# Kernel optimization log

Measured on AMD Instinct MI355X. Metric: run time of the kernel, lower is better.

The kernel has to match this reference:

```python
import jax, jax.numpy as jnp
import numpy as np

T, B, H, IN = 512, 128, 1024, 64  # IN = input_dim (x_feat=63 plus 1 feedback channel)
INIT_OUT = 1e-9


def setup_inputs() -> dict:
    key = jax.random.key(0)
    ks = jax.random.split(key, 8)
    s_ih = 1.0 / np.sqrt(H)
    return {
        "x": jax.random.normal(ks[0], (T, B, IN - 1), dtype=jnp.float32),
        # torch nn.LSTM params, gate order i,f,g,o stacked along dim 0
        "W_ih": jax.random.uniform(ks[1], (4 * H, IN), dtype=jnp.float32, minval=-s_ih, maxval=s_ih),
        "W_hh": jax.random.uniform(ks[2], (4 * H, H), dtype=jnp.float32, minval=-s_ih, maxval=s_ih),
        "b_ih": jax.random.uniform(ks[3], (4 * H,), dtype=jnp.float32, minval=-s_ih, maxval=s_ih),
        "b_hh": jax.random.uniform(ks[4], (4 * H,), dtype=jnp.float32, minval=-s_ih, maxval=s_ih),
        # nn.Linear(hidden_dim, 1)
        "W_lin": jax.random.uniform(ks[5], (1, H), dtype=jnp.float32, minval=-s_ih, maxval=s_ih),
        "b_lin": jax.random.uniform(ks[6], (1,), dtype=jnp.float32, minval=-s_ih, maxval=s_ih),
    }


def _forward(x, W_ih, W_hh, b_ih, b_hh, W_lin, b_lin):
    b = b_ih + b_hh

    def step(carry, xt):
        h, c, prev_out = carry  # h,c: (B,H); prev_out: (B,)
        inp = jnp.concatenate([xt, prev_out[:, None]], axis=1)  # (B, IN)
        gates = inp @ W_ih.T + h @ W_hh.T + b                   # (B, 4H)
        i, f, g, o = jnp.split(gates, 4, axis=1)
        c = jax.nn.sigmoid(f) * c + jax.nn.sigmoid(i) * jnp.tanh(g)
        h = jax.nn.sigmoid(o) * jnp.tanh(c)
        out = (h @ W_lin.T + b_lin)[:, 0]                        # (B,)
        return (h, c, out), out

    h0 = jnp.zeros((B, H), x.dtype)
    c0 = jnp.zeros((B, H), x.dtype)
    out0 = jnp.full((B,), INIT_OUT, x.dtype)
    _, outs = jax.lax.scan(step, (h0, c0, out0), x[1:])          # (T-1, B)
    return jnp.concatenate([out0[None, :], outs], axis=0)        # (T, B)


def reference(x, W_ih, W_hh, b_ih, b_hh, W_lin, b_lin):
    return _forward(x, W_ih, W_hh, b_ih, b_hh, W_lin, b_lin)
```

## Files before the change

### kernel.cpp

```cpp
#include <hip/hip_runtime.h>
#include <stdint.h>


typedef short short8 __attribute__((ext_vector_type(8)));
typedef float float4v __attribute__((ext_vector_type(4)));
typedef int int4v __attribute__((ext_vector_type(4)));

#define KP 1152

__device__ __forceinline__ unsigned short f2bf(float f) {
  unsigned int u = __float_as_uint(f);
  u += 0x7fffu + ((u >> 16) & 1u);
  return (unsigned short)(u >> 16);
}
__device__ __forceinline__ float sigm(float x) { return 1.0f / (1.0f + __expf(-x)); }
__device__ __forceinline__ float tanh_f(float x) {
  float ax = fabsf(x);
  float e = __expf(-2.0f * ax);
  float r = (1.0f - e) / (1.0f + e);
  return x < 0.0f ? -r : r;
}

__global__ void prep_w(const float* __restrict__ W_ih, const float* __restrict__ W_hh,
                       const float* __restrict__ W_lin, const float* __restrict__ b_ih,
                       const float* __restrict__ b_hh, const float* __restrict__ b_lin,
                       unsigned short* __restrict__ Wcat, float* __restrict__ b1,
                       float* __restrict__ b2) {
  int idx = blockIdx.x * 256 + threadIdx.x;
  if (idx < 4096 * KP) {
    int j = idx / KP;
    int k = idx - j * KP;
    float v = 0.0f;
    if (k < 63) v = W_ih[j * 64 + k];
    else if (k >= 64 && k < 1088) {
      int kk = k - 64;
      v = W_hh[j * 1024 + kk] + W_ih[j * 64 + 63] * W_lin[kk];
    }
    Wcat[idx] = f2bf(v);
  }
  if (idx < 4096) {
    float wfb = W_ih[idx * 64 + 63];
    float base = b_ih[idx] + b_hh[idx];
    b1[idx] = base + 1e-9f * wfb;
    b2[idx] = base + b_lin[0] * wfb;
  }
}

__global__ void prep_x(const float* __restrict__ x, unsigned short* __restrict__ xbf) {
  int idx = blockIdx.x * 256 + threadIdx.x;
  int c = idx & 63;
  int bi = idx >> 6;
  unsigned short v = 0;
  if (c < 63) v = f2bf(x[bi * 63 + c]);
  xbf[idx] = v;
}

__global__ void initk(unsigned int* __restrict__ Hz, int* __restrict__ flags) {
  int idx = blockIdx.x * 256 + threadIdx.x;
  Hz[idx] = 0u;
  Hz[idx + 65536] = 0u;
  if (idx < 1024) flags[idx] = 0;
}

__global__ __launch_bounds__(256, 1) void lstm_rec(
    const unsigned short* __restrict__ Wcat, const unsigned short* __restrict__ xbf,
    const float* __restrict__ b1, const float* __restrict__ b2,
    const float* __restrict__ Wlin, unsigned short* __restrict__ Hbuf,
    float* __restrict__ outp, int* __restrict__ flags) {
  const int tid = threadIdx.x;
  const int bid = blockIdx.x;
  const int g = bid & 7;
  const int mb = bid >> 3;
  const int wv = tid >> 6;
  const int ln = tid & 63;
  const int lr = ln & 15;
  const int lq = ln >> 4;
  const int rp = wv * 2 + (ln >> 5);
  const int c = ln & 31;

  __shared__ __align__(16) float pbuf[2][4][8][16][20];

  short8 bf[8][9];
#pragma unroll
  for (int n = 0; n < 8; ++n) {
    const unsigned short* wrow =
        Wcat + (size_t)((n >> 1) * 1024 + mb * 32 + (n & 1) * 16 + lr) * KP;
#pragma unroll
    for (int j = 0; j < 9; ++j)
      bf[n][j] = *reinterpret_cast<const short8*>(wrow + (wv * 9 + j) * 32 + lq * 8);
  }
#pragma unroll
  for (int n = 0; n < 8; ++n)
#pragma unroll
    for (int j = 0; j < 9; ++j)
      asm volatile("" : "+v"(bf[n][j]));

  const int kb = wv * 9;
  const int jlo = (kb < 2) ? 2 : 0;
  const int jhi = (kb + 9 > 34) ? 7 : 9;
  const int pmin = (kb < 2) ? 0 : kb - 2;
  const int pmax = (kb + 6 < 31) ? kb + 6 : 31;
  const int cnt = 4 * (pmax - pmin + 1);
  const int* fp = flags + g * 128 + 4 * pmin + ((ln < cnt) ? ln : cnt - 1);

  int hoff[9];
#pragma unroll
  for (int j = 0; j < 9; ++j)
    hoff[j] = ((g * 16 + lr) * 1024 + (kb + j - 2) * 32 + lq * 8) * 2;

  const int gcb = mb * 32 + c;
  float bias2[4];
#pragma unroll
  for (int q = 0; q < 4; ++q) bias2[q] = b2[q * 1024 + gcb];
  const float wl = Wlin[gcb];
  float cs0 = 0.f, cs1 = 0.f;

  for (int t = 1; t < 512; ++t) {
    const int tm1 = t - 1;
    short8 xa0, xa1;
    if (kb == 0) {
      const unsigned short* xrow =
          xbf + (size_t)t * 8192 + (g * 16 + lr) * 64 + lq * 8;
      xa0 = *reinterpret_cast<const short8*>(xrow);
      xa1 = *reinterpret_cast<const short8*>(xrow + 32);
    }

    if (t > 1) {
      int guard = 0;
      for (;;) {
        int v;
        asm volatile("global_load_dword %0, %1, off sc0 sc1\n\ts_waitcnt vmcnt(0)"
                     : "=v"(v) : "v"(fp) : "memory");
        if (__all(v >= tm1)) break;
        if (++guard > (1 << 18)) break;
      }
    }

    const unsigned short* hb = Hbuf + ((t - 1) & 1) * 131072;
    short8 af[9];
    if (kb == 0) { af[0] = xa0; af[1] = xa1; }
    if (jhi == 7) {
      short8 z8 = {0, 0, 0, 0, 0, 0, 0, 0};
      af[7] = z8; af[8] = z8;
    }
#pragma unroll
    for (int j = 0; j < 9; ++j)
      if (j >= jlo && j < jhi)
        asm volatile("global_load_dwordx4 %0, %1, %2 sc0 sc1"
                     : "=v"(af[j]) : "v"(hoff[j]), "s"(hb));
    asm volatile("s_waitcnt vmcnt(0)" ::: "memory");
    __builtin_amdgcn_sched_barrier(0);

    float4v acc[8];
#pragma unroll
    for (int n = 0; n < 8; ++n) acc[n] = (float4v){0.f, 0.f, 0.f, 0.f};
#pragma unroll
    for (int j = 0; j < 9; ++j)
#pragma unroll
      for (int n = 0; n < 8; ++n)
        acc[n] = __builtin_amdgcn_mfma_f32_16x16x32_bf16(af[j], bf[n][j], acc[n], 0, 0, 0);

#pragma unroll
    for (int n = 0; n < 8; ++n)
      *reinterpret_cast<float4v*>(&pbuf[t & 1][wv][n][lr][lq * 4]) = acc[n];
    __syncthreads();

    float ga0[4], ga1[4];
    const int nlo = c >> 4;
    const int cc = c & 15;
#pragma unroll
    for (int q = 0; q < 4; ++q) {
      float s0 = 0.f, s1 = 0.f;
#pragma unroll
      for (int w2 = 0; w2 < 4; ++w2) {
        const float* pp = &pbuf[t & 1][w2][q * 2 + nlo][cc][2 * rp];
        s0 += pp[0];
        s1 += pp[1];
      }
      ga0[q] = s0;
      ga1[q] = s1;
    }
    float lb0 = bias2[0], lb1 = bias2[1], lb2 = bias2[2], lb3 = bias2[3];
    if (t == 1) {
      lb0 = b1[gcb];
      lb1 = b1[1024 + gcb];
      lb2 = b1[2048 + gcb];
      lb3 = b1[3072 + gcb];
    }
    float i0 = sigm(ga0[0] + lb0), f0 = sigm(ga0[1] + lb1);
    float G0 = tanh_f(ga0[2] + lb2), o0 = sigm(ga0[3] + lb3);
    float i1 = sigm(ga1[0] + lb0), f1 = sigm(ga1[1] + lb1);
    float G1 = tanh_f(ga1[2] + lb2), o1 = sigm(ga1[3] + lb3);
    cs0 = f0 * cs0 + i0 * G0;
    cs1 = f1 * cs1 + i1 * G1;
    float h0v = o0 * tanh_f(cs0);
    float h1v = o1 * tanh_f(cs1);

    unsigned short* Hd = Hbuf + (t & 1) * 131072;
    const int r0 = g * 16 + rp * 2;
    unsigned short* p0 = Hd + (size_t)r0 * 1024 + gcb;
    unsigned short* p1 = p0 + 1024;
    int hb0 = (int)f2bf(h0v), hb1 = (int)f2bf(h1v);
    asm volatile("global_store_short %0, %1, off sc0 sc1" :: "v"(p0), "v"(hb0) : "memory");
    asm volatile("global_store_short %0, %1, off sc0 sc1" :: "v"(p1), "v"(hb1) : "memory");
    asm volatile("s_waitcnt vmcnt(0)" ::: "memory");
    if (ln == 0) {
      int* fp2 = flags + g * 128 + mb * 4 + wv;
      asm volatile("global_store_dword %0, %1, off sc0 sc1" :: "v"(fp2), "v"(t) : "memory");
    }

    float pa = h0v * wl, pb = h1v * wl;
    pa += __shfl_xor(pa, 1); pb += __shfl_xor(pb, 1);
    pa += __shfl_xor(pa, 2); pb += __shfl_xor(pb, 2);
    pa += __shfl_xor(pa, 4); pb += __shfl_xor(pb, 4);
    pa += __shfl_xor(pa, 8); pb += __shfl_xor(pb, 8);
    pa += __shfl_xor(pa, 16); pb += __shfl_xor(pb, 16);
    if (c == 0) {
      outp[(size_t)(t * 128 + r0) * 32 + mb] = pa;
      outp[(size_t)(t * 128 + r0 + 1) * 32 + mb] = pb;
    }
  }
}

__global__ void finalize(const float* __restrict__ outp, const float* __restrict__ b_lin,
                         float* __restrict__ out) {
  int tid = threadIdx.x;
  int ln = tid & 63;
  int wv = tid >> 6;
  int half = ln >> 5;
  int lane = ln & 31;
  int row = blockIdx.x * 8 + wv * 2 + half;
  float v = outp[(size_t)row * 32 + lane];
  v += __shfl_xor(v, 1);
  v += __shfl_xor(v, 2);
  v += __shfl_xor(v, 4);
  v += __shfl_xor(v, 8);
  v += __shfl_xor(v, 16);
  if (lane == 0) out[row] = (row < 128) ? 1e-9f : (v + b_lin[0]);
}

extern "C" void kernel_launch(void* const* d_in, const int* in_sizes, int n_in,
                              void* d_out, int out_size, void* d_ws, size_t ws_size,
                              hipStream_t stream) {
  const float* x = (const float*)d_in[0];
  const float* W_ih = (const float*)d_in[1];
  const float* W_hh = (const float*)d_in[2];
  const float* b_ih = (const float*)d_in[3];
  const float* b_hh = (const float*)d_in[4];
  const float* W_lin = (const float*)d_in[5];
  const float* b_lin = (const float*)d_in[6];
  float* out = (float*)d_out;

  char* ws = (char*)d_ws;
  const size_t WS_WCAT = 0;
  const size_t WS_XBF  = 9437184;
  const size_t WS_B1   = 17825792;
  const size_t WS_B2   = 17842176;
  const size_t WS_H    = 17858560;
  const size_t WS_OUTP = 18382848;
  const size_t WS_FLAG = 26771456;
  if (ws_size < WS_FLAG + 4096) return;

  unsigned short* Wcat = (unsigned short*)(ws + WS_WCAT);
  unsigned short* xbf = (unsigned short*)(ws + WS_XBF);
  float* b1 = (float*)(ws + WS_B1);
  float* b2 = (float*)(ws + WS_B2);
  unsigned short* Hbuf = (unsigned short*)(ws + WS_H);
  float* outp = (float*)(ws + WS_OUTP);
  int* flags = (int*)(ws + WS_FLAG);

  prep_w<<<18432, 256, 0, stream>>>(W_ih, W_hh, W_lin, b_ih, b_hh, b_lin, Wcat, b1, b2);
  prep_x<<<16384, 256, 0, stream>>>(x, xbf);
  initk<<<256, 256, 0, stream>>>((unsigned int*)Hbuf, flags);
  lstm_rec<<<256, 256, 0, stream>>>(Wcat, xbf, b1, b2, W_lin, Hbuf, outp, flags);
  finalize<<<8192, 256, 0, stream>>>(outp, b_lin, out);
}
```

Baseline: 2.086 ms.

## Split recurrent LSTM kernel across 512 blocks with 16 hidden columns each

Halves the hidden-column slice per block (16 instead of 32) and launches 512 persistent blocks at two per CU instead of 256 at one. Each wave then holds half the weight fragments and issues half the MFMAs per step, so two co-resident blocks can overlap each other's latency and spin-waits. The flag array doubles and pollers read two flags per lane. The partial-output buffer widens to 64 slices, with finalize adjusted to match. This relies on all 512 blocks being co-resident for the spin barrier and adds more flag traffic per step.

```diff
diff --git a/kernel.cpp b/kernel.cpp
--- a/kernel.cpp
+++ b/kernel.cpp
@@ -5,6 +5,7 @@
 typedef short short8 __attribute__((ext_vector_type(8)));
 typedef float float4v __attribute__((ext_vector_type(4)));
 typedef int int4v __attribute__((ext_vector_type(4)));
+typedef int int2v __attribute__((ext_vector_type(2)));
 
 #define KP 1152
 
@@ -59,10 +60,10 @@
   int idx = blockIdx.x * 256 + threadIdx.x;
   Hz[idx] = 0u;
   Hz[idx + 65536] = 0u;
-  if (idx < 1024) flags[idx] = 0;
-}
-
-__global__ __launch_bounds__(256, 1) void lstm_rec(
+  if (idx < 2048) flags[idx] = 0;
+}
+
+__global__ __launch_bounds__(256, 2) void lstm_rec(
     const unsigned short* __restrict__ Wcat, const unsigned short* __restrict__ xbf,
     const float* __restrict__ b1, const float* __restrict__ b2,
     const float* __restrict__ Wlin, unsigned short* __restrict__ Hbuf,
@@ -75,22 +76,21 @@
   const int ln = tid & 63;
   const int lr = ln & 15;
   const int lq = ln >> 4;
-  const int rp = wv * 2 + (ln >> 5);
-  const int c = ln & 31;
-
-  __shared__ __align__(16) float pbuf[2][4][8][16][20];
-
-  short8 bf[8][9];
-#pragma unroll
-  for (int n = 0; n < 8; ++n) {
-    const unsigned short* wrow =
-        Wcat + (size_t)((n >> 1) * 1024 + mb * 32 + (n & 1) * 16 + lr) * KP;
+  const int prow = tid >> 4;
+  const int pcol = tid & 15;
+
+  __shared__ __align__(16) float pbuf[2][4][4][16][20];
+
+  short8 bf[4][9];
+#pragma unroll
+  for (int n = 0; n < 4; ++n) {
+    const unsigned short* wrow = Wcat + (size_t)(n * 1024 + mb * 16 + lr) * KP;
 #pragma unroll
     for (int j = 0; j < 9; ++j)
       bf[n][j] = *reinterpret_cast<const short8*>(wrow + (wv * 9 + j) * 32 + lq * 8);
   }
 #pragma unroll
-  for (int n = 0; n < 8; ++n)
+  for (int n = 0; n < 4; ++n)
 #pragma unroll
     for (int j = 0; j < 9; ++j)
       asm volatile("" : "+v"(bf[n][j]));
@@ -98,22 +98,23 @@
   const int kb = wv * 9;
   const int jlo = (kb < 2) ? 2 : 0;
   const int jhi = (kb + 9 > 34) ? 7 : 9;
-  const int pmin = (kb < 2) ? 0 : kb - 2;
-  const int pmax = (kb + 6 < 31) ? kb + 6 : 31;
-  const int cnt = 4 * (pmax - pmin + 1);
-  const int* fp = flags + g * 128 + 4 * pmin + ((ln < cnt) ? ln : cnt - 1);
+  const int cmin = (kb < 2) ? 0 : kb - 2;
+  const int cmax = (kb + 6 < 31) ? kb + 6 : 31;
+  const int cnt = 8 * (cmax - cmin + 1);
+  const int half = cnt >> 1;
+  const int* fp = flags + g * 256 + 8 * cmin + 2 * ((ln < half) ? ln : half - 1);
 
   int hoff[9];
 #pragma unroll
   for (int j = 0; j < 9; ++j)
     hoff[j] = ((g * 16 + lr) * 1024 + (kb + j - 2) * 32 + lq * 8) * 2;
 
-  const int gcb = mb * 32 + c;
+  const int gcb = mb * 16 + pcol;
   float bias2[4];
 #pragma unroll
   for (int q = 0; q < 4; ++q) bias2[q] = b2[q * 1024 + gcb];
   const float wl = Wlin[gcb];
-  float cs0 = 0.f, cs1 = 0.f;
+  float cs = 0.f;
 
   for (int t = 1; t < 512; ++t) {
     const int tm1 = t - 1;
@@ -128,10 +129,10 @@
     if (t > 1) {
       int guard = 0;
       for (;;) {
-        int v;
-        asm volatile("global_load_dword %0, %1, off sc0 sc1\n\ts_waitcnt vmcnt(0)"
-                     : "=v"(v) : "v"(fp) : "memory");
-        if (__all(v >= tm1)) break;
+        int2v ff;
+        asm volatile("global_load_dwordx2 %0, %1, off sc0 sc1\n\ts_waitcnt vmcnt(0)"
+                     : "=v"(ff) : "v"(fp) : "memory");
+        if (__all((ff.x >= tm1) && (ff.y >= tm1))) break;
         if (++guard > (1 << 18)) break;
       }
     }
@@ -151,34 +152,25 @@
     asm volatile("s_waitcnt vmcnt(0)" ::: "memory");
     __builtin_amdgcn_sched_barrier(0);
 
-    float4v acc[8];
-#pragma unroll
-    for (int n = 0; n < 8; ++n) acc[n] = (float4v){0.f, 0.f, 0.f, 0.f};
-#pragma unroll
-    for (int j = 0; j < 9; ++j)
-#pragma unroll
-      for (int n = 0; n < 8; ++n)
+    float4v acc[4];
+#pragma unroll
+    for (int n = 0; n < 4; ++n) acc[n] = (float4v){0.f, 0.f, 0.f, 0.f};
+#pragma unroll
+    for (int j = 0; j < 9; ++j)
+#pragma unroll
+      for (int n = 0; n < 4; ++n)
         acc[n] = __builtin_amdgcn_mfma_f32_16x16x32_bf16(af[j], bf[n][j], acc[n], 0, 0, 0);
 
 #pragma unroll
-    for (int n = 0; n < 8; ++n)
+    for (int n = 0; n < 4; ++n)
       *reinterpret_cast<float4v*>(&pbuf[t & 1][wv][n][lr][lq * 4]) = acc[n];
     __syncthreads();
 
-    float ga0[4], ga1[4];
-    const int nlo = c >> 4;
-    const int cc = c & 15;
+    float ga[4];
 #pragma unroll
     for (int q = 0; q < 4; ++q) {
-      float s0 = 0.f, s1 = 0.f;
-#pragma unroll
-      for (int w2 = 0; w2 < 4; ++w2) {
-        const float* pp = &pbuf[t & 1][w2][q * 2 + nlo][cc][2 * rp];
-        s0 += pp[0];
-        s1 += pp[1];
-      }
-      ga0[q] = s0;
-      ga1[q] = s1;
+      const float* pp0 = &pbuf[t & 1][0][q][pcol][prow];
+      ga[q] = pp0[0] + pp0[4 * 16 * 20] + pp0[2 * 4 * 16 * 20] + pp0[3 * 4 * 16 * 20];
     }
     float lb0 = bias2[0], lb1 = bias2[1], lb2 = bias2[2], lb3 = bias2[3];
     if (t == 1) {
@@ -187,38 +179,28 @@
       lb2 = b1[2048 + gcb];
       lb3 = b1[3072 + gcb];
     }
-    float i0 = sigm(ga0[0] + lb0), f0 = sigm(ga0[1] + lb1);
-    float G0 = tanh_f(ga0[2] + lb2), o0 = sigm(ga0[3] + lb3);
-    float i1 = sigm(ga1[0] + lb0), f1 = sigm(ga1[1] + lb1);
-    float G1 = tanh_f(ga1[2] + lb2), o1 = sigm(ga1[3] + lb3);
-    cs0 = f0 * cs0 + i0 * G0;
-    cs1 = f1 * cs1 + i1 * G1;
-    float h0v = o0 * tanh_f(cs0);
-    float h1v = o1 * tanh_f(cs1);
+    float iv = sigm(ga[0] + lb0), fv = sigm(ga[1] + lb1);
+    float Gv = tanh_f(ga[2] + lb2), ov = sigm(ga[3] + lb3);
+    cs = fv * cs + iv * Gv;
+    float hv = ov * tanh_f(cs);
 
     unsigned short* Hd = Hbuf + (t & 1) * 131072;
-    const int r0 = g * 16 + rp * 2;
-    unsigned short* p0 = Hd + (size_t)r0 * 1024 + gcb;
-    unsigned short* p1 = p0 + 1024;
-    int hb0 = (int)f2bf(h0v), hb1 = (int)f2bf(h1v);
+    unsigned short* p0 = Hd + (size_t)(g * 16 + prow) * 1024 + gcb;
+    int hb0 = (int)f2bf(hv);
     asm volatile("global_store_short %0, %1, off sc0 sc1" :: "v"(p0), "v"(hb0) : "memory");
-    asm volatile("global_store_short %0, %1, off sc0 sc1" :: "v"(p1), "v"(hb1) : "memory");
     asm volatile("s_waitcnt vmcnt(0)" ::: "memory");
     if (ln == 0) {
-      int* fp2 = flags + g * 128 + mb * 4 + wv;
+      int* fp2 = flags + g * 256 + mb * 4 + wv;
       asm volatile("global_store_dword %0, %1, off sc0 sc1" :: "v"(fp2), "v"(t) : "memory");
     }
 
-    float pa = h0v * wl, pb = h1v * wl;
-    pa += __shfl_xor(pa, 1); pb += __shfl_xor(pb, 1);
-    pa += __shfl_xor(pa, 2); pb += __shfl_xor(pb, 2);
-    pa += __shfl_xor(pa, 4); pb += __shfl_xor(pb, 4);
-    pa += __shfl_xor(pa, 8); pb += __shfl_xor(pb, 8);
-    pa += __shfl_xor(pa, 16); pb += __shfl_xor(pb, 16);
-    if (c == 0) {
-      outp[(size_t)(t * 128 + r0) * 32 + mb] = pa;
-      outp[(size_t)(t * 128 + r0 + 1) * 32 + mb] = pb;
-    }
+    float pa = hv * wl;
+    pa += __shfl_xor(pa, 1);
+    pa += __shfl_xor(pa, 2);
+    pa += __shfl_xor(pa, 4);
+    pa += __shfl_xor(pa, 8);
+    if (pcol == 0)
+      outp[(size_t)(t * 128 + g * 16 + prow) * 64 + mb] = pa;
   }
 }
 
@@ -227,16 +209,15 @@
   int tid = threadIdx.x;
   int ln = tid & 63;
   int wv = tid >> 6;
-  int half = ln >> 5;
-  int lane = ln & 31;
-  int row = blockIdx.x * 8 + wv * 2 + half;
-  float v = outp[(size_t)row * 32 + lane];
+  int row = blockIdx.x * 4 + wv;
+  float v = outp[(size_t)row * 64 + ln];
   v += __shfl_xor(v, 1);
   v += __shfl_xor(v, 2);
   v += __shfl_xor(v, 4);
   v += __shfl_xor(v, 8);
   v += __shfl_xor(v, 16);
-  if (lane == 0) out[row] = (row < 128) ? 1e-9f : (v + b_lin[0]);
+  v += __shfl_xor(v, 32);
+  if (ln == 0) out[row] = (row < 128) ? 1e-9f : (v + b_lin[0]);
 }
 
 extern "C" void kernel_launch(void* const* d_in, const int* in_sizes, int n_in,
@@ -258,8 +239,8 @@
   const size_t WS_B2   = 17842176;
   const size_t WS_H    = 17858560;
   const size_t WS_OUTP = 18382848;
-  const size_t WS_FLAG = 26771456;
-  if (ws_size < WS_FLAG + 4096) return;
+  const size_t WS_END  = 35160064;
+  if (ws_size < WS_END) return;
 
   unsigned short* Wcat = (unsigned short*)(ws + WS_WCAT);
   unsigned short* xbf = (unsigned short*)(ws + WS_XBF);
@@ -267,11 +248,11 @@
   float* b2 = (float*)(ws + WS_B2);
   unsigned short* Hbuf = (unsigned short*)(ws + WS_H);
   float* outp = (float*)(ws + WS_OUTP);
-  int* flags = (int*)(ws + WS_FLAG);
+  int* flags = (int*)(ws + WS_OUTP);
 
   prep_w<<<18432, 256, 0, stream>>>(W_ih, W_hh, W_lin, b_ih, b_hh, b_lin, Wcat, b1, b2);
   prep_x<<<16384, 256, 0, stream>>>(x, xbf);
   initk<<<256, 256, 0, stream>>>((unsigned int*)Hbuf, flags);
-  lstm_rec<<<256, 256, 0, stream>>>(Wcat, xbf, b1, b2, W_lin, Hbuf, outp, flags);
-  finalize<<<8192, 256, 0, stream>>>(outp, b_lin, out);
-}
+  lstm_rec<<<512, 256, 0, stream>>>(Wcat, xbf, b1, b2, W_lin, Hbuf, outp, flags);
+  finalize<<<16384, 256, 0, stream>>>(outp, b_lin, out);
+}
```

Result: slower. 4.371 ms (+109.5%).

## Retile LSTM recurrence to 32-row batch groups with LDS-resident weight slices

Applied to the files above, without the earlier changes.

Changes the persistent recurrent kernel's work split. Each of the 256 blocks now covers 32 batch rows by 16 hidden columns across all four gates, instead of 16 rows by 32 columns. Most W_hh tiles move into shared memory, with the input weights and tail tiles kept in registers. Each B fragment read from LDS now feeds two MFMAs, one per 16-row half, which is meant to cut weight register pressure and make better use of each loaded weight. The cost is per-step LDS reads, more hidden-state loads per block, a second barrier per step, and a wider partial-output buffer that shares workspace with the flag array.

```diff
diff --git a/kernel.cpp b/kernel.cpp
--- a/kernel.cpp
+++ b/kernel.cpp
@@ -69,60 +69,83 @@
     float* __restrict__ outp, int* __restrict__ flags) {
   const int tid = threadIdx.x;
   const int bid = blockIdx.x;
-  const int g = bid & 7;
-  const int mb = bid >> 3;
+  const int g = bid & 3;
+  const int mb = bid >> 2;
   const int wv = tid >> 6;
   const int ln = tid & 63;
   const int lr = ln & 15;
   const int lq = ln >> 4;
-  const int rp = wv * 2 + (ln >> 5);
-  const int c = ln & 31;
-
-  __shared__ __align__(16) float pbuf[2][4][8][16][20];
-
-  short8 bf[8][9];
-#pragma unroll
-  for (int n = 0; n < 8; ++n) {
-    const unsigned short* wrow =
-        Wcat + (size_t)((n >> 1) * 1024 + mb * 32 + (n & 1) * 16 + lr) * KP;
-#pragma unroll
-    for (int j = 0; j < 9; ++j)
-      bf[n][j] = *reinterpret_cast<const short8*>(wrow + (wv * 9 + j) * 32 + lq * 8);
+  const int rp = tid >> 4;
+  const int pcol = tid & 15;
+
+  __shared__ __align__(16) char wlds[122880];
+  __shared__ __align__(16) float pbuf[4][4][2][16][18];
+
+  const int hb = wv * 8;
+
+  short8 xw[4];
+  short8 rw[2][4];
+  {
+    const unsigned short* wbase = Wcat + (size_t)(mb * 16 + lr) * KP;
+#pragma unroll
+    for (int jj = 0; jj < 8; ++jj) {
+      int ht = hb + jj;
+      if (ht < 30) {
+#pragma unroll
+        for (int n = 0; n < 4; ++n) {
+          short8 v = *reinterpret_cast<const short8*>(
+              wbase + (size_t)n * 1024 * KP + 64 + ht * 32 + lq * 8);
+          *reinterpret_cast<short8*>(wlds + ((ht * 4 + n) << 10) + ln * 16) = v;
+        }
+      }
+    }
+    if (wv < 2) {
+#pragma unroll
+      for (int n = 0; n < 4; ++n) {
+        xw[n] = *reinterpret_cast<const short8*>(
+            wbase + (size_t)n * 1024 * KP + wv * 32 + lq * 8);
+        asm volatile("" : "+v"(xw[n]));
+      }
+    }
+    if (wv == 3) {
+#pragma unroll
+      for (int k = 0; k < 2; ++k)
+#pragma unroll
+        for (int n = 0; n < 4; ++n) {
+          rw[k][n] = *reinterpret_cast<const short8*>(
+              wbase + (size_t)n * 1024 * KP + 64 + (30 + k) * 32 + lq * 8);
+          asm volatile("" : "+v"(rw[k][n]));
+        }
+    }
   }
-#pragma unroll
-  for (int n = 0; n < 8; ++n)
-#pragma unroll
-    for (int j = 0; j < 9; ++j)
-      asm volatile("" : "+v"(bf[n][j]));
-
-  const int kb = wv * 9;
-  const int jlo = (kb < 2) ? 2 : 0;
-  const int jhi = (kb + 9 > 34) ? 7 : 9;
-  const int pmin = (kb < 2) ? 0 : kb - 2;
-  const int pmax = (kb + 6 < 31) ? kb + 6 : 31;
-  const int cnt = 4 * (pmax - pmin + 1);
-  const int* fp = flags + g * 128 + 4 * pmin + ((ln < cnt) ? ln : cnt - 1);
-
-  int hoff[9];
-#pragma unroll
-  for (int j = 0; j < 9; ++j)
-    hoff[j] = ((g * 16 + lr) * 1024 + (kb + j - 2) * 32 + lq * 8) * 2;
-
-  const int gcb = mb * 32 + c;
+  __syncthreads();
+
+  const int* fp = flags + g * 256 + wv * 64 + ln;
+
+  int hoff[8][2];
+#pragma unroll
+  for (int j = 0; j < 8; ++j)
+#pragma unroll
+    for (int m = 0; m < 2; ++m)
+      hoff[j][m] = ((g * 32 + m * 16 + lr) * 1024 + (hb + j) * 32 + lq * 8) * 2;
+
+  const int gcb = mb * 16 + pcol;
   float bias2[4];
 #pragma unroll
   for (int q = 0; q < 4; ++q) bias2[q] = b2[q * 1024 + gcb];
   const float wl = Wlin[gcb];
+  const int m_pw = rp >> 3;
+  const int r16 = (rp & 7) * 2;
   float cs0 = 0.f, cs1 = 0.f;
 
   for (int t = 1; t < 512; ++t) {
     const int tm1 = t - 1;
-    short8 xa0, xa1;
-    if (kb == 0) {
-      const unsigned short* xrow =
-          xbf + (size_t)t * 8192 + (g * 16 + lr) * 64 + lq * 8;
-      xa0 = *reinterpret_cast<const short8*>(xrow);
-      xa1 = *reinterpret_cast<const short8*>(xrow + 32);
+    short8 ax0, ax1;
+    if (wv < 2) {
+      const unsigned short* xr =
+          xbf + (size_t)t * 8192 + (g * 32 + lr) * 64 + wv * 32 + lq * 8;
+      ax0 = *reinterpret_cast<const short8*>(xr);
+      ax1 = *reinterpret_cast<const short8*>(xr + 16 * 64);
     }
 
     if (t > 1) {
@@ -136,50 +159,72 @@
       }
     }
 
-    const unsigned short* hb = Hbuf + ((t - 1) & 1) * 131072;
-    short8 af[9];
-    if (kb == 0) { af[0] = xa0; af[1] = xa1; }
-    if (jhi == 7) {
-      short8 z8 = {0, 0, 0, 0, 0, 0, 0, 0};
-      af[7] = z8; af[8] = z8;
-    }
-#pragma unroll
-    for (int j = 0; j < 9; ++j)
-      if (j >= jlo && j < jhi)
+    const unsigned short* hbase = Hbuf + ((t - 1) & 1) * 131072;
+    short8 af[8][2];
+#pragma unroll
+    for (int j = 0; j < 8; ++j)
+#pragma unroll
+      for (int m = 0; m < 2; ++m)
         asm volatile("global_load_dwordx4 %0, %1, %2 sc0 sc1"
-                     : "=v"(af[j]) : "v"(hoff[j]), "s"(hb));
+                     : "=v"(af[j][m]) : "v"(hoff[j][m]), "s"(hbase));
     asm volatile("s_waitcnt vmcnt(0)" ::: "memory");
     __builtin_amdgcn_sched_barrier(0);
 
-    float4v acc[8];
-#pragma unroll
-    for (int n = 0; n < 8; ++n) acc[n] = (float4v){0.f, 0.f, 0.f, 0.f};
-#pragma unroll
-    for (int j = 0; j < 9; ++j)
-#pragma unroll
-      for (int n = 0; n < 8; ++n)
-        acc[n] = __builtin_amdgcn_mfma_f32_16x16x32_bf16(af[j], bf[n][j], acc[n], 0, 0, 0);
-
-#pragma unroll
-    for (int n = 0; n < 8; ++n)
-      *reinterpret_cast<float4v*>(&pbuf[t & 1][wv][n][lr][lq * 4]) = acc[n];
+    float4v acc[4][2];
+#pragma unroll
+    for (int n = 0; n < 4; ++n) {
+      acc[n][0] = (float4v){0.f, 0.f, 0.f, 0.f};
+      acc[n][1] = (float4v){0.f, 0.f, 0.f, 0.f};
+    }
+    if (wv < 2) {
+#pragma unroll
+      for (int n = 0; n < 4; ++n) {
+        acc[n][0] = __builtin_amdgcn_mfma_f32_16x16x32_bf16(ax0, xw[n], acc[n][0], 0, 0, 0);
+        acc[n][1] = __builtin_amdgcn_mfma_f32_16x16x32_bf16(ax1, xw[n], acc[n][1], 0, 0, 0);
+      }
+    }
+#pragma unroll
+    for (int j = 0; j < 8; ++j) {
+      short8 bf0, bf1, bf2, bf3;
+      if (hb + j < 30) {
+        const char* p = wlds + (((hb + j) * 4) << 10) + ln * 16;
+        bf0 = *reinterpret_cast<const short8*>(p);
+        bf1 = *reinterpret_cast<const short8*>(p + 1024);
+        bf2 = *reinterpret_cast<const short8*>(p + 2048);
+        bf3 = *reinterpret_cast<const short8*>(p + 3072);
+      } else {
+        bf0 = rw[hb + j - 30][0];
+        bf1 = rw[hb + j - 30][1];
+        bf2 = rw[hb + j - 30][2];
+        bf3 = rw[hb + j - 30][3];
+      }
+      acc[0][0] = __builtin_amdgcn_mfma_f32_16x16x32_bf16(af[j][0], bf0, acc[0][0], 0, 0, 0);
+      acc[0][1] = __builtin_amdgcn_mfma_f32_16x16x32_bf16(af[j][1], bf0, acc[0][1], 0, 0, 0);
+      acc[1][0] = __builtin_amdgcn_mfma_f32_16x16x32_bf16(af[j][0], bf1, acc[1][0], 0, 0, 0);
+      acc[1][1] = __builtin_amdgcn_mfma_f32_16x16x32_bf16(af[j][1], bf1, acc[1][1], 0, 0, 0);
+      acc[2][0] = __builtin_amdgcn_mfma_f32_16x16x32_bf16(af[j][0], bf2, acc[2][0], 0, 0, 0);
+      acc[2][1] = __builtin_amdgcn_mfma_f32_16x16x32_bf16(af[j][1], bf2, acc[2][1], 0, 0, 0);
+      acc[3][0] = __builtin_amdgcn_mfma_f32_16x16x32_bf16(af[j][0], bf3, acc[3][0], 0, 0, 0);
+      acc[3][1] = __builtin_amdgcn_mfma_f32_16x16x32_bf16(af[j][1], bf3, acc[3][1], 0, 0, 0);
+    }
+
+#pragma unroll
+    for (int n = 0; n < 4; ++n)
+#pragma unroll
+      for (int m = 0; m < 2; ++m)
+        *reinterpret_cast<float4v*>(&pbuf[wv][n][m][lr][lq * 4]) = acc[n][m];
     __syncthreads();
 
     float ga0[4], ga1[4];
-    const int nlo = c >> 4;
-    const int cc = c & 15;
 #pragma unroll
     for (int q = 0; q < 4; ++q) {
-      float s0 = 0.f, s1 = 0.f;
-#pragma unroll
-      for (int w2 = 0; w2 < 4; ++w2) {
-        const float* pp = &pbuf[t & 1][w2][q * 2 + nlo][cc][2 * rp];
-        s0 += pp[0];
-        s1 += pp[1];
-      }
-      ga0[q] = s0;
-      ga1[q] = s1;
-    }
+      ga0[q] = pbuf[0][q][m_pw][pcol][r16] + pbuf[1][q][m_pw][pcol][r16] +
+               pbuf[2][q][m_pw][pcol][r16] + pbuf[3][q][m_pw][pcol][r16];
+      ga1[q] = pbuf[0][q][m_pw][pcol][r16 + 1] + pbuf[1][q][m_pw][pcol][r16 + 1] +
+               pbuf[2][q][m_pw][pcol][r16 + 1] + pbuf[3][q][m_pw][pcol][r16 + 1];
+    }
+    __syncthreads();
+
     float lb0 = bias2[0], lb1 = bias2[1], lb2 = bias2[2], lb3 = bias2[3];
     if (t == 1) {
       lb0 = b1[gcb];
@@ -196,16 +241,16 @@
     float h0v = o0 * tanh_f(cs0);
     float h1v = o1 * tanh_f(cs1);
 
+    const int grow = g * 32 + 2 * rp;
     unsigned short* Hd = Hbuf + (t & 1) * 131072;
-    const int r0 = g * 16 + rp * 2;
-    unsigned short* p0 = Hd + (size_t)r0 * 1024 + gcb;
+    unsigned short* p0 = Hd + (size_t)grow * 1024 + gcb;
     unsigned short* p1 = p0 + 1024;
     int hb0 = (int)f2bf(h0v), hb1 = (int)f2bf(h1v);
     asm volatile("global_store_short %0, %1, off sc0 sc1" :: "v"(p0), "v"(hb0) : "memory");
     asm volatile("global_store_short %0, %1, off sc0 sc1" :: "v"(p1), "v"(hb1) : "memory");
     asm volatile("s_waitcnt vmcnt(0)" ::: "memory");
     if (ln == 0) {
-      int* fp2 = flags + g * 128 + mb * 4 + wv;
+      int* fp2 = flags + g * 256 + mb * 4 + wv;
       asm volatile("global_store_dword %0, %1, off sc0 sc1" :: "v"(fp2), "v"(t) : "memory");
     }
 
@@ -214,10 +259,9 @@
     pa += __shfl_xor(pa, 2); pb += __shfl_xor(pb, 2);
     pa += __shfl_xor(pa, 4); pb += __shfl_xor(pb, 4);
     pa += __shfl_xor(pa, 8); pb += __shfl_xor(pb, 8);
-    pa += __shfl_xor(pa, 16); pb += __shfl_xor(pb, 16);
-    if (c == 0) {
-      outp[(size_t)(t * 128 + r0) * 32 + mb] = pa;
-      outp[(size_t)(t * 128 + r0 + 1) * 32 + mb] = pb;
+    if (pcol == 0) {
+      outp[(size_t)(t * 128 + grow) * 64 + mb] = pa;
+      outp[(size_t)(t * 128 + grow + 1) * 64 + mb] = pb;
     }
   }
 }
@@ -227,16 +271,15 @@
   int tid = threadIdx.x;
   int ln = tid & 63;
   int wv = tid >> 6;
-  int half = ln >> 5;
-  int lane = ln & 31;
-  int row = blockIdx.x * 8 + wv * 2 + half;
-  float v = outp[(size_t)row * 32 + lane];
+  int row = blockIdx.x * 4 + wv;
+  float v = outp[(size_t)row * 64 + ln];
   v += __shfl_xor(v, 1);
   v += __shfl_xor(v, 2);
   v += __shfl_xor(v, 4);
   v += __shfl_xor(v, 8);
   v += __shfl_xor(v, 16);
-  if (lane == 0) out[row] = (row < 128) ? 1e-9f : (v + b_lin[0]);
+  v += __shfl_xor(v, 32);
+  if (ln == 0) out[row] = (row < 128) ? 1e-9f : (v + b_lin[0]);
 }
 
 extern "C" void kernel_launch(void* const* d_in, const int* in_sizes, int n_in,
@@ -258,8 +301,8 @@
   const size_t WS_B2   = 17842176;
   const size_t WS_H    = 17858560;
   const size_t WS_OUTP = 18382848;
-  const size_t WS_FLAG = 26771456;
-  if (ws_size < WS_FLAG + 4096) return;
+  const size_t WS_END  = 35160064;
+  if (ws_size < WS_END) return;
 
   unsigned short* Wcat = (unsigned short*)(ws + WS_WCAT);
   unsigned short* xbf = (unsigned short*)(ws + WS_XBF);
@@ -267,11 +310,11 @@
   float* b2 = (float*)(ws + WS_B2);
   unsigned short* Hbuf = (unsigned short*)(ws + WS_H);
   float* outp = (float*)(ws + WS_OUTP);
-  int* flags = (int*)(ws + WS_FLAG);
+  int* flags = (int*)(ws + WS_OUTP);
 
   prep_w<<<18432, 256, 0, stream>>>(W_ih, W_hh, W_lin, b_ih, b_hh, b_lin, Wcat, b1, b2);
   prep_x<<<16384, 256, 0, stream>>>(x, xbf);
   initk<<<256, 256, 0, stream>>>((unsigned int*)Hbuf, flags);
   lstm_rec<<<256, 256, 0, stream>>>(Wcat, xbf, b1, b2, W_lin, Hbuf, outp, flags);
-  finalize<<<8192, 256, 0, stream>>>(outp, b_lin, out);
-}
+  finalize<<<16384, 256, 0, stream>>>(outp, b_lin, out);
+}
```

After: 3.338 ms. 1.6x slower.
